# Optimization experiments

Hardware: AMD Instinct MI355X
Metric: run time of the kernel (lower is better)

Reference implementation:

```python
import jax, jax.numpy as jnp
import numpy as np

B, T, N = 2, 256, 512
H, S, C = 64, 8, 8
DYN = 4


def setup_inputs() -> dict:
    key = jax.random.key(0)
    ks = jax.random.split(key, 12)
    sc = 0.05
    return {
        "x": jax.random.normal(ks[0], (B, T, N), jnp.float32),
        "mask": (jax.random.uniform(ks[1], (B, T, N)) < 0.2).astype(jnp.float32),
        "static_context": jax.random.normal(ks[2], (N, S), jnp.float32),
        "node_coords": jax.random.normal(ks[3], (N, C), jnp.float32),
        "W1": jax.random.normal(ks[4], (DYN + S, H), jnp.float32) * sc,
        "b1": jnp.zeros((H,), jnp.float32),
        "W2": jax.random.normal(ks[5], (H, H), jnp.float32) * sc,
        "b2": jnp.zeros((H,), jnp.float32),
        "We1": jax.random.normal(ks[6], (4 * H, H), jnp.float32) * sc,
        "be1": jnp.zeros((H,), jnp.float32),
        "We2": jax.random.normal(ks[7], (H, 1), jnp.float32) * sc,
        "be2": jnp.zeros((1,), jnp.float32),
        "self_loop_logit": jnp.float32(0.5),
        "prior_strength": jnp.float32(1.0),
        "similarity_strength": jnp.float32(1.0),
        "temperature": jnp.float32(0.7),
    }


def reference(x, mask, static_context, node_coords, W1, b1, W2, b2,
              We1, be1, We2, be2, self_loop_logit, prior_strength,
              similarity_strength, temperature):
    Bv, Tv, Nv = x.shape
    # ---- dynamic per-node context over time ----
    observed = 1.0 - mask                                   # [B,T,N]
    count = jnp.maximum(observed.sum(axis=1), 1.0)          # [B,N]
    mean = (x * observed).sum(axis=1) / count               # [B,N]
    centered = (x - mean[:, None, :]) * observed
    std = jnp.sqrt((centered ** 2).sum(axis=1) / count + 1e-6)
    t_idx = jnp.arange(Tv, dtype=x.dtype)[None, :, None]
    latest = jnp.argmax(t_idx * observed, axis=1)           # [B,N] int
    last = jnp.take_along_axis(x, latest[:, None, :], axis=1)[:, 0, :]
    missing_ratio = mask.mean(axis=1)
    dyn = jnp.stack([mean, std, last, missing_ratio], axis=-1)  # [B,N,4]
    # ---- node encoder ----
    static = jnp.broadcast_to(static_context[None], (Bv, Nv, static_context.shape[-1]))
    feats = jnp.concatenate([dyn, static], axis=-1)
    h = jax.nn.relu(feats @ W1 + b1)
    h = jax.nn.relu(h @ W2 + b2)                            # [B,N,H]
    hn = h / jnp.maximum(jnp.linalg.norm(h, axis=-1, keepdims=True), 1e-12)
    # ---- edge MLP on pair features [h_i, h_j, |h_i-h_j|, h_i*h_j] ----
    # split first-layer weight into the four blocks so h_i/h_j terms are O(N)
    Wi, Wj, Wa, Wp = jnp.split(We1, 4, axis=0)              # each [H,H]
    pre_i = h @ Wi                                          # [B,N,H]
    pre_j = h @ Wj
    hi = h[:, :, None, :]                                   # [B,N,1,H]
    hj = h[:, None, :, :]                                   # [B,1,N,H]
    hidden = jax.nn.relu(pre_i[:, :, None, :] + pre_j[:, None, :, :]
                         + jnp.abs(hi - hj) @ Wa + (hi * hj) @ Wp + be1)
    edge_logits = (hidden @ We2 + be2)[..., 0]              # [B,N,N]
    # ---- cosine similarity + distance prior ----
    cos = jnp.einsum('bnh,bmh->bnm', hn, hn)
    eye = jnp.eye(Nv, dtype=x.dtype)
    off = 1.0 - eye
    diff = node_coords[:, None, :] - node_coords[None, :, :]
    dist = jnp.sqrt(jnp.maximum((diff ** 2).sum(-1), 1e-12))
    prior = (1.0 / (1.0 + dist)) * off                      # [N,N]
    # ---- combine, softmax, symmetrize, row-normalize ----
    logits = (edge_logits * off
              + jax.nn.softplus(prior_strength) * prior[None]
              + jax.nn.softplus(similarity_strength) * (cos * off))
    logits = logits + eye[None] * jax.nn.softplus(self_loop_logit)
    temp = jax.nn.softplus(temperature) + 1e-4
    adj = jax.nn.softmax(logits / temp, axis=-1)
    adj = 0.5 * (adj + jnp.swapaxes(adj, -1, -2))
    adj = adj / jnp.maximum(adj.sum(axis=-1, keepdims=True), 1e-6)
    return adj
```

## Files before the change

### kernel.cpp

```cpp
#include <hip/hip_runtime.h>
#include <hip/hip_bf16.h>
#include <math.h>

#define NB 2
#define NT 256
#define NN 512
#define NH 64
#define NS 8
#define NC 8

#define OFF_H      0
#define OFF_PVEC   65536
#define OFF_HF16   131072
#define OFF_HNF16  163840
#define OFF_WA16   196608
#define OFF_WJF    198656
#define OFF_WPF    202752
#define OFF_GBASE  206848
#define OFF_UNSYM  731136

typedef __attribute__((ext_vector_type(8))) _Float16 h8;
typedef __attribute__((ext_vector_type(2))) __fp16 fp16x2;
typedef __attribute__((ext_vector_type(4))) float f32x4;
typedef __attribute__((ext_vector_type(4))) unsigned u4;
typedef __attribute__((ext_vector_type(2))) unsigned u2;

__device__ __forceinline__ float softplusf(float x){
  if (x > 20.f) return x;
  return log1pf(expf(x));
}

__device__ __forceinline__ unsigned pkh(float a, float b){
  fp16x2 h = __builtin_amdgcn_cvt_pkrtz(a, b);
  return __builtin_bit_cast(unsigned, h);
}

template<int CTRL>
__device__ __forceinline__ float dpp_addf(float x){
  int xi = __builtin_bit_cast(int, x);
  int yi = __builtin_amdgcn_update_dpp(0, xi, CTRL, 0xF, 0xF, true);
  return x + __builtin_bit_cast(float, yi);
}
__device__ __forceinline__ float row16_sum(float x){
  x = dpp_addf<0xB1>(x);
  x = dpp_addf<0x4E>(x);
  x = dpp_addf<0x141>(x);
  x = dpp_addf<0x140>(x);
  return x;
}

__global__ __launch_bounds__(256) void k_front(
    const float* __restrict__ x, const float* __restrict__ mask,
    const float* __restrict__ sctx,
    const float* __restrict__ W1, const float* __restrict__ b1,
    const float* __restrict__ W2, const float* __restrict__ b2,
    const float* __restrict__ We1, const float* __restrict__ be1,
    float* __restrict__ hg, float* __restrict__ pvec,
    unsigned* __restrict__ hf16, unsigned* __restrict__ hn16,
    short* __restrict__ wa16, float* __restrict__ wjf,
    float* __restrict__ wpf){
  int blk = blockIdx.x;
  int tid = threadIdx.x;

  if (blk >= 256){
    int pidx = (blk - 256)*256 + tid;
    int e    = pidx & 7;
    int lane = (pidx >> 3) & 63;
    int frag = (pidx >> 9) & 7;
    int nt = frag & 3, ks = frag >> 2;
    int kg = lane >> 4, q = lane & 15;
    int kk = ks*32 + kg*8 + e;
    int c  = nt*16 + q;
    if (pidx < 4096){
      _Float16 v = (_Float16)We1[(128 + kk)*NH + c];
      wa16[pidx] = __builtin_bit_cast(short, v);
    } else if (pidx < 8192){
      wjf[pidx - 4096] = We1[(64 + kk)*NH + c];
    } else {
      wpf[pidx - 8192] = We1[(192 + kk)*NH + c];
    }
    return;
  }

  int b  = blk >> 7;
  int n0 = (blk & 127) * 4;

  int nl = tid & 3;
  int ts = tid >> 2;
  int n  = n0 + nl;

  float cnt = 0.f, sx = 0.f, sxx = 0.f;
  int lastt = 0;
  for (int t = ts*4; t < ts*4 + 4; ++t){
    int idx = (b*NT + t)*NN + n;
    float xv = x[idx];
    float mv = mask[idx];
    bool obs = (mv < 0.5f);
    if (obs){ cnt += 1.f; sx += xv; sxx += xv*xv; lastt = t; }
  }
  #pragma unroll
  for (int m = 4; m < 64; m <<= 1){
    cnt   += __shfl_xor(cnt,  m);
    sx    += __shfl_xor(sx,   m);
    sxx   += __shfl_xor(sxx,  m);
    lastt  = max(lastt, __shfl_xor(lastt, m));
  }
  int w = tid >> 6;
  __shared__ float r_cnt[4][4], r_sx[4][4], r_sxx[4][4];
  __shared__ int   r_lt[4][4];
  __shared__ float s_dyn[4][4];
  if ((tid & 63) < 4){
    r_cnt[w][nl] = cnt; r_sx[w][nl] = sx; r_sxx[w][nl] = sxx; r_lt[w][nl] = lastt;
  }
  __syncthreads();
  if (tid < 4){
    float c = 0.f, s1 = 0.f, s2 = 0.f; int lt = 0;
    #pragma unroll
    for (int ww = 0; ww < 4; ++ww){
      c  += r_cnt[ww][tid]; s1 += r_sx[ww][tid]; s2 += r_sxx[ww][tid];
      lt  = max(lt, r_lt[ww][tid]);
    }
    float cc   = fmaxf(c, 1.f);
    float mean = s1 / cc;
    float var  = s2 / cc - mean*mean;
    float stdv = sqrtf(fmaxf(var, 0.f) + 1e-6f);
    float last = x[(b*NT + lt)*NN + n0 + tid];
    float mr   = 1.f - c * (1.f/(float)NT);
    s_dyn[tid][0] = mean; s_dyn[tid][1] = stdv; s_dyn[tid][2] = last; s_dyn[tid][3] = mr;
  }
  __syncthreads();

  int c = tid & 63;
  int gn = n0 + w;
  int bn = b*NN + gn;
  __shared__ float s_f[4][12];
  __shared__ float s_h1[4][64];
  __shared__ float s_h2[4][64];

  if (c < 4)       s_f[w][c] = s_dyn[w][c];
  else if (c < 12) s_f[w][c] = sctx[gn*NS + (c-4)];
  __syncthreads();

  float a = b1[c];
  #pragma unroll
  for (int k = 0; k < 12; ++k) a = fmaf(s_f[w][k], W1[k*NH + c], a);
  s_h1[w][c] = fmaxf(a, 0.f);
  __syncthreads();

  float a2 = b2[c];
  #pragma unroll 8
  for (int k = 0; k < 64; ++k) a2 = fmaf(s_h1[w][k], W2[k*NH + c], a2);
  a2 = fmaxf(a2, 0.f);

  float sq = a2*a2;
  #pragma unroll
  for (int m = 1; m < 64; m <<= 1) sq += __shfl_xor(sq, m);
  float inv = 1.f / fmaxf(sqrtf(sq), 1e-12f);

  s_h2[w][c] = a2;
  __syncthreads();

  float pi = be1[c];
  #pragma unroll 8
  for (int k = 0; k < 64; ++k) pi = fmaf(s_h2[w][k], We1[k*NH + c], pi);

  hg  [bn*64 + c] = a2;
  pvec[bn*64 + c] = pi;
  if (c < 32){
    float e0 = s_h2[w][2*c], e1 = s_h2[w][2*c + 1];
    hf16[bn*32 + c] = pkh(e0, e1);
    hn16[bn*32 + c] = pkh(e0*inv, e1*inv);
  }
}

__global__ __launch_bounds__(256) void k_gram(
    const unsigned* __restrict__ hn16, const float* __restrict__ s_ss,
    float* __restrict__ gbase){
  int b   = blockIdx.x;
  int i0  = blockIdx.y * 16;
  int jq  = blockIdx.z;
  int tid = threadIdx.x;
  int w   = tid >> 6;
  int lane = tid & 63;
  float spss = softplusf(s_ss[0]);

  const u4* hv = (const u4*)hn16;
  int arow = i0 + (lane & 15);
  u4 a0 = hv[(b*NN + arow)*8 + (lane >> 4)];
  u4 a1 = hv[(b*NN + arow)*8 + (lane >> 4) + 4];
  h8 A0 = __builtin_bit_cast(h8, a0);
  h8 A1 = __builtin_bit_cast(h8, a1);

  #pragma unroll
  for (int t = 0; t < 2; ++t){
    int j0 = (jq*8 + w*2 + t) * 16;
    int jrow = j0 + (lane & 15);
    u4 b0 = hv[(b*NN + jrow)*8 + (lane >> 4)];
    u4 b1 = hv[(b*NN + jrow)*8 + (lane >> 4) + 4];
    f32x4 acc = (f32x4){0.f, 0.f, 0.f, 0.f};
    acc = __builtin_amdgcn_mfma_f32_16x16x32_f16(A0, __builtin_bit_cast(h8, b0), acc, 0, 0, 0);
    acc = __builtin_amdgcn_mfma_f32_16x16x32_f16(A1, __builtin_bit_cast(h8, b1), acc, 0, 0, 0);
    #pragma unroll
    for (int r = 0; r < 4; ++r){
      int irow = i0 + (lane >> 4)*4 + r;
      gbase[(size_t)(b*NN + irow)*NN + j0 + (lane & 15)] = spss * acc[r];
    }
  }
}

__global__ __launch_bounds__(512, 4) void k_logits(
    const float* __restrict__ hg, const float* __restrict__ pvec,
    const unsigned* __restrict__ hf16, const short* __restrict__ wa16,
    const float* __restrict__ wjf, const float* __restrict__ wpf,
    const float* __restrict__ coords, const float* __restrict__ We2,
    const float* __restrict__ be2, const float* __restrict__ gbase,
    const float* __restrict__ s_sl, const float* __restrict__ s_ps,
    const float* __restrict__ s_tp,
    float* __restrict__ unsym){
  int blk = blockIdx.x;
  int b = blk >> 9, i = blk & (NN-1);
  int tid  = threadIdx.x;
  int w    = tid >> 6;
  int lane = tid & 63;
  int q    = lane & 15;
  int kg   = lane >> 4;

  __shared__ __align__(16) float s_hi[64];
  __shared__ __align__(16) float s_pv[64];
  __shared__ __align__(16) float s_prior[NN];
  __shared__ __align__(16) float s_gcos[NN];
  __shared__ __align__(16) float lrow[NN];
  __shared__ __align__(16) unsigned lds_wa[2048];
  __shared__ __align__(16) unsigned lds_cw[2048];
  __shared__ __align__(16) unsigned s_hj[8][16*34 + 2];
  __shared__ float red[16];

  float spsl = softplusf(s_sl[0]);
  float spps = softplusf(s_ps[0]);
  float invt = 1.f / (softplusf(s_tp[0]) + 1e-4f);

  if (tid < 64){
    s_hi[tid] = hg  [(b*NN + i)*64 + tid];
    s_pv[tid] = pvec[(b*NN + i)*64 + tid];
  }
  {
    int j = tid;
    float4 ci0 = *(const float4*)(coords + i*NC);
    float4 ci1 = *(const float4*)(coords + i*NC + 4);
    float4 cj0 = *(const float4*)(coords + j*NC);
    float4 cj1 = *(const float4*)(coords + j*NC + 4);
    float dd = 0.f;
    dd = fmaf(ci0.x-cj0.x, ci0.x-cj0.x, dd);
    dd = fmaf(ci0.y-cj0.y, ci0.y-cj0.y, dd);
    dd = fmaf(ci0.z-cj0.z, ci0.z-cj0.z, dd);
    dd = fmaf(ci0.w-cj0.w, ci0.w-cj0.w, dd);
    dd = fmaf(ci1.x-cj1.x, ci1.x-cj1.x, dd);
    dd = fmaf(ci1.y-cj1.y, ci1.y-cj1.y, dd);
    dd = fmaf(ci1.z-cj1.z, ci1.z-cj1.z, dd);
    dd = fmaf(ci1.w-cj1.w, ci1.w-cj1.w, dd);
    float dist = sqrtf(fmaxf(dd, 1e-12f));
    s_prior[j] = (j == i) ? 0.f : spps / (1.f + dist);
    s_gcos[j]  = gbase[(size_t)(b*NN + i)*NN + j];
  }
  __syncthreads();

  {
    int frag = tid >> 6;
    int l2   = tid & 63;
    const u4* wsrc = (const u4*)wa16;
    *(u4*)&lds_wa[(frag*64 + l2)*4] = wsrc[frag*64 + l2];

    int ch0 = (frag >> 2)*32 + (l2 >> 4)*8;
    const float* wj = wjf + (frag*64 + l2)*8;
    const float* wp = wpf + (frag*64 + l2)*8;
    u4 u;
    #pragma unroll
    for (int d = 0; d < 4; ++d){
      float v0 = fmaf(s_hi[ch0 + 2*d],     wp[2*d],     wj[2*d]);
      float v1 = fmaf(s_hi[ch0 + 2*d + 1], wp[2*d + 1], wj[2*d + 1]);
      u[d] = pkh(v0, v1);
    }
    *(u4*)&lds_cw[(frag*64 + l2)*4] = u;
  }

  const u4* hfv = (const u4*)hf16;
  u4 hi0 = hfv[(b*NN + i)*8 + kg];
  u4 hi1 = hfv[(b*NN + i)*8 + kg + 4];

  float pv4[4], we2q[4];
  #pragma unroll
  for (int nt = 0; nt < 4; ++nt){
    pv4[nt]  = pvec[(b*NN + i)*64 + nt*16 + q];
    we2q[nt] = We2[nt*16 + q];
  }
  float be2v = be2[0];
  __syncthreads();

  unsigned* slice = &s_hj[w][0];
  const u4 absm = (u4){0x7fff7fffu, 0x7fff7fffu, 0x7fff7fffu, 0x7fff7fffu};

  #pragma unroll
  for (int s = 0; s < 4; ++s){
    int it = w + s*8;
    int jbase = it * 16;

    {
      int r8 = lane >> 3, c8 = lane & 7;
      u4 g0 = *(const u4*)((const unsigned*)hf16 + (size_t)(b*NN + jbase + r8)*32 + c8*4);
      u4 g1 = *(const u4*)((const unsigned*)hf16 + (size_t)(b*NN + jbase + 8 + r8)*32 + c8*4);
      unsigned* p0 = slice + r8*34 + c8*4;
      unsigned* p1 = slice + (8 + r8)*34 + c8*4;
      u2 t;
      t.x = g0.x; t.y = g0.y; *(u2*)p0 = t;
      t.x = g0.z; t.y = g0.w; *(u2*)(p0 + 2) = t;
      t.x = g1.x; t.y = g1.y; *(u2*)p1 = t;
      t.x = g1.z; t.y = g1.w; *(u2*)(p1 + 2) = t;
    }

    u4 hj0, hj1;
    {
      unsigned* rp = slice + q*34 + kg*4;
      u2 a0 = *(u2*)rp;
      u2 a1 = *(u2*)(rp + 2);
      u2 b0 = *(u2*)(rp + 16);
      u2 b1 = *(u2*)(rp + 18);
      hj0.x = a0.x; hj0.y = a0.y; hj0.z = a1.x; hj0.w = a1.y;
      hj1.x = b0.x; hj1.y = b0.y; hj1.z = b1.x; hj1.w = b1.y;
    }

    h8 dh0 = __builtin_bit_cast(h8, hi0) - __builtin_bit_cast(h8, hj0);
    h8 dh1 = __builtin_bit_cast(h8, hi1) - __builtin_bit_cast(h8, hj1);
    h8 af0 = __builtin_bit_cast(h8, __builtin_bit_cast(u4, dh0) & absm);
    h8 af1 = __builtin_bit_cast(h8, __builtin_bit_cast(u4, dh1) & absm);
    h8 af2 = __builtin_bit_cast(h8, hj0);
    h8 af3 = __builtin_bit_cast(h8, hj1);

    f32x4 acc[4];
    #pragma unroll
    for (int nt = 0; nt < 4; ++nt)
      acc[nt] = (f32x4){pv4[nt], pv4[nt], pv4[nt], pv4[nt]};
    #pragma unroll
    for (int nt = 0; nt < 4; ++nt){
      h8 wA0 = __builtin_bit_cast(h8, *(const u4*)&lds_wa[((0*4 + nt)*64 + lane)*4]);
      h8 wA1 = __builtin_bit_cast(h8, *(const u4*)&lds_wa[((1*4 + nt)*64 + lane)*4]);
      h8 wC0 = __builtin_bit_cast(h8, *(const u4*)&lds_cw[((0*4 + nt)*64 + lane)*4]);
      h8 wC1 = __builtin_bit_cast(h8, *(const u4*)&lds_cw[((1*4 + nt)*64 + lane)*4]);
      acc[nt] = __builtin_amdgcn_mfma_f32_16x16x32_f16(af0, wA0, acc[nt], 0, 0, 0);
      acc[nt] = __builtin_amdgcn_mfma_f32_16x16x32_f16(af1, wA1, acc[nt], 0, 0, 0);
      acc[nt] = __builtin_amdgcn_mfma_f32_16x16x32_f16(af2, wC0, acc[nt], 0, 0, 0);
      acc[nt] = __builtin_amdgcn_mfma_f32_16x16x32_f16(af3, wC1, acc[nt], 0, 0, 0);
    }

    float part[4] = {0.f, 0.f, 0.f, 0.f};
    #pragma unroll
    for (int nt = 0; nt < 4; ++nt)
      #pragma unroll
      for (int r = 0; r < 4; ++r)
        part[r] = fmaf(fmaxf(acc[nt][r], 0.f), we2q[nt], part[r]);
    #pragma unroll
    for (int r = 0; r < 4; ++r) part[r] = row16_sum(part[r]);

    if (q < 4){
      int j2 = jbase + kg*4 + q;
      float ps2 = part[0];
      ps2 = (q == 1) ? part[1] : ps2;
      ps2 = (q == 2) ? part[2] : ps2;
      ps2 = (q == 3) ? part[3] : ps2;
      float lg = ps2 + be2v + s_prior[j2] + s_gcos[j2];
      lrow[j2] = (j2 == i) ? spsl : lg;
    }
  }
  __syncthreads();

  float v = lrow[tid];
  float m1 = v;
  #pragma unroll
  for (int msk = 1; msk < 64; msk <<= 1) m1 = fmaxf(m1, __shfl_xor(m1, msk));
  if (lane == 0) red[w] = m1;
  __syncthreads();
  m1 = red[0];
  #pragma unroll
  for (int ww = 1; ww < 8; ++ww) m1 = fmaxf(m1, red[ww]);

  float e = expf((v - m1) * invt);
  float se = e;
  #pragma unroll
  for (int msk = 1; msk < 64; msk <<= 1) se += __shfl_xor(se, msk);
  if (lane == 0) red[8 + w] = se;
  __syncthreads();
  se = red[8];
  #pragma unroll
  for (int ww = 1; ww < 8; ++ww) se += red[8 + ww];

  unsym[(size_t)(b*NN + i)*NN + tid] = e / se;
}

__global__ __launch_bounds__(256) void k_sym(
    const float* __restrict__ u, float* __restrict__ out){
  int blk = blockIdx.x;
  int b = blk >> 9, i = blk & (NN-1);
  int tid = threadIdx.x;
  const float* urow = u + (size_t)(b*NN + i) * NN;
  float v0, v1, rs;
  {
    int j0 = tid, j1 = tid + 256;
    float a1 = urow[j0];
    float a2 = u[(size_t)(b*NN + j0) * NN + i];
    v0 = 0.5f*(a1 + a2);
    float a3 = urow[j1];
    float a4 = u[(size_t)(b*NN + j1) * NN + i];
    v1 = 0.5f*(a3 + a4);
    rs = v0 + v1;
  }
  int lane = tid & 63, w = tid >> 6;
  #pragma unroll
  for (int msk = 1; msk < 64; msk <<= 1) rs += __shfl_xor(rs, msk);
  __shared__ float red[4];
  if (lane == 0) red[w] = rs;
  __syncthreads();
  rs = red[0] + red[1] + red[2] + red[3];
  float inv = 1.f / fmaxf(rs, 1e-6f);
  float* orow = out + (size_t)(b*NN + i) * NN;
  orow[tid]       = v0 * inv;
  orow[tid + 256] = v1 * inv;
}

extern "C" void kernel_launch(void* const* d_in, const int* in_sizes, int n_in,
                              void* d_out, int out_size, void* d_ws, size_t ws_size,
                              hipStream_t stream){
  const float* x      = (const float*)d_in[0];
  const float* mask   = (const float*)d_in[1];
  const float* sctx   = (const float*)d_in[2];
  const float* coords = (const float*)d_in[3];
  const float* W1     = (const float*)d_in[4];
  const float* b1     = (const float*)d_in[5];
  const float* W2     = (const float*)d_in[6];
  const float* b2     = (const float*)d_in[7];
  const float* We1    = (const float*)d_in[8];
  const float* be1    = (const float*)d_in[9];
  const float* We2    = (const float*)d_in[10];
  const float* be2    = (const float*)d_in[11];
  const float* sl     = (const float*)d_in[12];
  const float* ps     = (const float*)d_in[13];
  const float* ss     = (const float*)d_in[14];
  const float* tp     = (const float*)d_in[15];

  float*    ws    = (float*)d_ws;
  float*    hgp   = ws + OFF_H;
  float*    pvecp = ws + OFF_PVEC;
  unsigned* hf16p = (unsigned*)(ws + OFF_HF16);
  unsigned* hn16p = (unsigned*)(ws + OFF_HNF16);
  short*    wa16p = (short*)(ws + OFF_WA16);
  float*    wjfp  = ws + OFF_WJF;
  float*    wpfp  = ws + OFF_WPF;
  float*    gbase = ws + OFF_GBASE;
  float*    unsym = ws + OFF_UNSYM;
  float*    out   = (float*)d_out;

  k_front <<<304, 256, 0, stream>>>(x, mask, sctx, W1, b1, W2, b2, We1, be1,
                                    hgp, pvecp, hf16p, hn16p, wa16p, wjfp, wpfp);
  k_gram  <<<dim3(NB, 32, 4), 256, 0, stream>>>(hn16p, ss, gbase);
  k_logits<<<NB*NN, 512, 0, stream>>>(hgp, pvecp, hf16p, wa16p, wjfp, wpfp,
                                      coords, We2, be2, gbase, sl, ps, tp, unsym);
  k_sym   <<<NB*NN, 256, 0, stream>>>(unsym, out);
}
```

Measured before the change: 46.29 us.

## Process two rows per logits block and precompute prior+bias in gram kernel

The logits kernel now handles two query rows per block. Each staged h_j tile and the shared Wa weight fragments are loaded once and reused for both rows, and the block count is halved. The distance prior and edge bias are moved into the gram kernel, which writes one combined additive term per (i,j), so the logits kernel no longer computes coordinates or reads two separate buffers. In exchange there are more registers (two accumulator sets) and more LDS per block, which may lower occupancy and parallelism on a 1024-row problem.

```diff
diff --git a/kernel.cpp b/kernel.cpp
--- a/kernel.cpp
+++ b/kernel.cpp
@@ -16,7 +16,7 @@
 #define OFF_WA16   196608
 #define OFF_WJF    198656
 #define OFF_WPF    202752
-#define OFF_GBASE  206848
+#define OFF_GEXT   206848
 #define OFF_UNSYM  731136
 
 typedef __attribute__((ext_vector_type(8))) _Float16 h8;
@@ -173,9 +173,10 @@
   }
 }
 
-__global__ __launch_bounds__(256) void k_gram(
-    const unsigned* __restrict__ hn16, const float* __restrict__ s_ss,
-    float* __restrict__ gbase){
+__global__ __launch_bounds__(256) void k_extra(
+    const unsigned* __restrict__ hn16, const float* __restrict__ coords,
+    const float* __restrict__ s_ss, const float* __restrict__ s_ps,
+    const float* __restrict__ be2, float* __restrict__ gext){
   int b   = blockIdx.x;
   int i0  = blockIdx.y * 16;
   int jq  = blockIdx.z;
@@ -183,6 +184,8 @@
   int w   = tid >> 6;
   int lane = tid & 63;
   float spss = softplusf(s_ss[0]);
+  float spps = softplusf(s_ps[0]);
+  float be2v = be2[0];
 
   const u4* hv = (const u4*)hn16;
   int arow = i0 + (lane & 15);
@@ -200,10 +203,27 @@
     f32x4 acc = (f32x4){0.f, 0.f, 0.f, 0.f};
     acc = __builtin_amdgcn_mfma_f32_16x16x32_f16(A0, __builtin_bit_cast(h8, b0), acc, 0, 0, 0);
     acc = __builtin_amdgcn_mfma_f32_16x16x32_f16(A1, __builtin_bit_cast(h8, b1), acc, 0, 0, 0);
+
+    int jc = j0 + (lane & 15);
+    float4 cj0 = *(const float4*)(coords + jc*NC);
+    float4 cj1 = *(const float4*)(coords + jc*NC + 4);
     #pragma unroll
     for (int r = 0; r < 4; ++r){
       int irow = i0 + (lane >> 4)*4 + r;
-      gbase[(size_t)(b*NN + irow)*NN + j0 + (lane & 15)] = spss * acc[r];
+      float4 ci0 = *(const float4*)(coords + irow*NC);
+      float4 ci1 = *(const float4*)(coords + irow*NC + 4);
+      float dd = 0.f;
+      dd = fmaf(ci0.x-cj0.x, ci0.x-cj0.x, dd);
+      dd = fmaf(ci0.y-cj0.y, ci0.y-cj0.y, dd);
+      dd = fmaf(ci0.z-cj0.z, ci0.z-cj0.z, dd);
+      dd = fmaf(ci0.w-cj0.w, ci0.w-cj0.w, dd);
+      dd = fmaf(ci1.x-cj1.x, ci1.x-cj1.x, dd);
+      dd = fmaf(ci1.y-cj1.y, ci1.y-cj1.y, dd);
+      dd = fmaf(ci1.z-cj1.z, ci1.z-cj1.z, dd);
+      dd = fmaf(ci1.w-cj1.w, ci1.w-cj1.w, dd);
+      float dist  = sqrtf(fmaxf(dd, 1e-12f));
+      float prior = (irow == jc) ? 0.f : spps / (1.f + dist);
+      gext[(size_t)(b*NN + irow)*NN + jc] = fmaf(spss, acc[r], be2v + prior);
     }
   }
 }
@@ -212,56 +232,34 @@
     const float* __restrict__ hg, const float* __restrict__ pvec,
     const unsigned* __restrict__ hf16, const short* __restrict__ wa16,
     const float* __restrict__ wjf, const float* __restrict__ wpf,
-    const float* __restrict__ coords, const float* __restrict__ We2,
-    const float* __restrict__ be2, const float* __restrict__ gbase,
-    const float* __restrict__ s_sl, const float* __restrict__ s_ps,
-    const float* __restrict__ s_tp,
+    const float* __restrict__ We2, const float* __restrict__ gext,
+    const float* __restrict__ s_sl, const float* __restrict__ s_tp,
     float* __restrict__ unsym){
   int blk = blockIdx.x;
-  int b = blk >> 9, i = blk & (NN-1);
+  int b  = blk >> 8;
+  int ip = (blk & 255) * 2;
   int tid  = threadIdx.x;
   int w    = tid >> 6;
   int lane = tid & 63;
   int q    = lane & 15;
   int kg   = lane >> 4;
 
-  __shared__ __align__(16) float s_hi[64];
-  __shared__ __align__(16) float s_pv[64];
-  __shared__ __align__(16) float s_prior[NN];
-  __shared__ __align__(16) float s_gcos[NN];
-  __shared__ __align__(16) float lrow[NN];
+  __shared__ __align__(16) float s_hi[2][64];
+  __shared__ __align__(16) float s_ext[2][NN];
+  __shared__ __align__(16) float lrow[2][NN];
   __shared__ __align__(16) unsigned lds_wa[2048];
-  __shared__ __align__(16) unsigned lds_cw[2048];
+  __shared__ __align__(16) unsigned lds_cw[2][2048];
   __shared__ __align__(16) unsigned s_hj[8][16*34 + 2];
-  __shared__ float red[16];
+  __shared__ float red[32];
 
   float spsl = softplusf(s_sl[0]);
-  float spps = softplusf(s_ps[0]);
   float invt = 1.f / (softplusf(s_tp[0]) + 1e-4f);
 
-  if (tid < 64){
-    s_hi[tid] = hg  [(b*NN + i)*64 + tid];
-    s_pv[tid] = pvec[(b*NN + i)*64 + tid];
-  }
-  {
-    int j = tid;
-    float4 ci0 = *(const float4*)(coords + i*NC);
-    float4 ci1 = *(const float4*)(coords + i*NC + 4);
-    float4 cj0 = *(const float4*)(coords + j*NC);
-    float4 cj1 = *(const float4*)(coords + j*NC + 4);
-    float dd = 0.f;
-    dd = fmaf(ci0.x-cj0.x, ci0.x-cj0.x, dd);
-    dd = fmaf(ci0.y-cj0.y, ci0.y-cj0.y, dd);
-    dd = fmaf(ci0.z-cj0.z, ci0.z-cj0.z, dd);
-    dd = fmaf(ci0.w-cj0.w, ci0.w-cj0.w, dd);
-    dd = fmaf(ci1.x-cj1.x, ci1.x-cj1.x, dd);
-    dd = fmaf(ci1.y-cj1.y, ci1.y-cj1.y, dd);
-    dd = fmaf(ci1.z-cj1.z, ci1.z-cj1.z, dd);
-    dd = fmaf(ci1.w-cj1.w, ci1.w-cj1.w, dd);
-    float dist = sqrtf(fmaxf(dd, 1e-12f));
-    s_prior[j] = (j == i) ? 0.f : spps / (1.f + dist);
-    s_gcos[j]  = gbase[(size_t)(b*NN + i)*NN + j];
-  }
+  if (tid < 128)
+    s_hi[tid >> 6][tid & 63] = hg[(b*NN + ip + (tid >> 6))*64 + (tid & 63)];
+  #pragma unroll
+  for (int r = 0; r < 2; ++r)
+    s_ext[r][tid] = gext[(size_t)(b*NN + ip + r)*NN + tid];
   __syncthreads();
 
   {
@@ -273,27 +271,35 @@
     int ch0 = (frag >> 2)*32 + (l2 >> 4)*8;
     const float* wj = wjf + (frag*64 + l2)*8;
     const float* wp = wpf + (frag*64 + l2)*8;
-    u4 u;
-    #pragma unroll
-    for (int d = 0; d < 4; ++d){
-      float v0 = fmaf(s_hi[ch0 + 2*d],     wp[2*d],     wj[2*d]);
-      float v1 = fmaf(s_hi[ch0 + 2*d + 1], wp[2*d + 1], wj[2*d + 1]);
-      u[d] = pkh(v0, v1);
-    }
-    *(u4*)&lds_cw[(frag*64 + l2)*4] = u;
+    #pragma unroll
+    for (int r = 0; r < 2; ++r){
+      u4 u;
+      #pragma unroll
+      for (int d = 0; d < 4; ++d){
+        float v0 = fmaf(s_hi[r][ch0 + 2*d],     wp[2*d],     wj[2*d]);
+        float v1 = fmaf(s_hi[r][ch0 + 2*d + 1], wp[2*d + 1], wj[2*d + 1]);
+        u[d] = pkh(v0, v1);
+      }
+      *(u4*)&lds_cw[r][(frag*64 + l2)*4] = u;
+    }
   }
 
   const u4* hfv = (const u4*)hf16;
-  u4 hi0 = hfv[(b*NN + i)*8 + kg];
-  u4 hi1 = hfv[(b*NN + i)*8 + kg + 4];
-
-  float pv4[4], we2q[4];
+  u4 hiA[2][2];
+  #pragma unroll
+  for (int r = 0; r < 2; ++r){
+    hiA[r][0] = hfv[(b*NN + ip + r)*8 + kg];
+    hiA[r][1] = hfv[(b*NN + ip + r)*8 + kg + 4];
+  }
+
+  float pv4[2][4], we2q[4];
   #pragma unroll
   for (int nt = 0; nt < 4; ++nt){
-    pv4[nt]  = pvec[(b*NN + i)*64 + nt*16 + q];
+    #pragma unroll
+    for (int r = 0; r < 2; ++r)
+      pv4[r][nt] = pvec[(b*NN + ip + r)*64 + nt*16 + q];
     we2q[nt] = We2[nt*16 + q];
   }
-  float be2v = be2[0];
   __syncthreads();
 
   unsigned* slice = &s_hj[w][0];
@@ -327,72 +333,94 @@
       hj0.x = a0.x; hj0.y = a0.y; hj0.z = a1.x; hj0.w = a1.y;
       hj1.x = b0.x; hj1.y = b0.y; hj1.z = b1.x; hj1.w = b1.y;
     }
-
-    h8 dh0 = __builtin_bit_cast(h8, hi0) - __builtin_bit_cast(h8, hj0);
-    h8 dh1 = __builtin_bit_cast(h8, hi1) - __builtin_bit_cast(h8, hj1);
-    h8 af0 = __builtin_bit_cast(h8, __builtin_bit_cast(u4, dh0) & absm);
-    h8 af1 = __builtin_bit_cast(h8, __builtin_bit_cast(u4, dh1) & absm);
-    h8 af2 = __builtin_bit_cast(h8, hj0);
-    h8 af3 = __builtin_bit_cast(h8, hj1);
-
-    f32x4 acc[4];
-    #pragma unroll
-    for (int nt = 0; nt < 4; ++nt)
-      acc[nt] = (f32x4){pv4[nt], pv4[nt], pv4[nt], pv4[nt]};
+    h8 hjv0 = __builtin_bit_cast(h8, hj0);
+    h8 hjv1 = __builtin_bit_cast(h8, hj1);
+
+    f32x4 acc[2][4];
+    #pragma unroll
+    for (int r = 0; r < 2; ++r)
+      #pragma unroll
+      for (int nt = 0; nt < 4; ++nt)
+        acc[r][nt] = (f32x4){pv4[r][nt], pv4[r][nt], pv4[r][nt], pv4[r][nt]};
+
     #pragma unroll
     for (int nt = 0; nt < 4; ++nt){
       h8 wA0 = __builtin_bit_cast(h8, *(const u4*)&lds_wa[((0*4 + nt)*64 + lane)*4]);
       h8 wA1 = __builtin_bit_cast(h8, *(const u4*)&lds_wa[((1*4 + nt)*64 + lane)*4]);
-      h8 wC0 = __builtin_bit_cast(h8, *(const u4*)&lds_cw[((0*4 + nt)*64 + lane)*4]);
-      h8 wC1 = __builtin_bit_cast(h8, *(const u4*)&lds_cw[((1*4 + nt)*64 + lane)*4]);
-      acc[nt] = __builtin_amdgcn_mfma_f32_16x16x32_f16(af0, wA0, acc[nt], 0, 0, 0);
-      acc[nt] = __builtin_amdgcn_mfma_f32_16x16x32_f16(af1, wA1, acc[nt], 0, 0, 0);
-      acc[nt] = __builtin_amdgcn_mfma_f32_16x16x32_f16(af2, wC0, acc[nt], 0, 0, 0);
-      acc[nt] = __builtin_amdgcn_mfma_f32_16x16x32_f16(af3, wC1, acc[nt], 0, 0, 0);
-    }
-
-    float part[4] = {0.f, 0.f, 0.f, 0.f};
-    #pragma unroll
-    for (int nt = 0; nt < 4; ++nt)
       #pragma unroll
-      for (int r = 0; r < 4; ++r)
-        part[r] = fmaf(fmaxf(acc[nt][r], 0.f), we2q[nt], part[r]);
-    #pragma unroll
-    for (int r = 0; r < 4; ++r) part[r] = row16_sum(part[r]);
-
-    if (q < 4){
-      int j2 = jbase + kg*4 + q;
-      float ps2 = part[0];
-      ps2 = (q == 1) ? part[1] : ps2;
-      ps2 = (q == 2) ? part[2] : ps2;
-      ps2 = (q == 3) ? part[3] : ps2;
-      float lg = ps2 + be2v + s_prior[j2] + s_gcos[j2];
-      lrow[j2] = (j2 == i) ? spsl : lg;
-    }
-  }
-  __syncthreads();
-
-  float v = lrow[tid];
-  float m1 = v;
-  #pragma unroll
-  for (int msk = 1; msk < 64; msk <<= 1) m1 = fmaxf(m1, __shfl_xor(m1, msk));
-  if (lane == 0) red[w] = m1;
-  __syncthreads();
-  m1 = red[0];
-  #pragma unroll
-  for (int ww = 1; ww < 8; ++ww) m1 = fmaxf(m1, red[ww]);
-
-  float e = expf((v - m1) * invt);
-  float se = e;
-  #pragma unroll
-  for (int msk = 1; msk < 64; msk <<= 1) se += __shfl_xor(se, msk);
-  if (lane == 0) red[8 + w] = se;
-  __syncthreads();
-  se = red[8];
-  #pragma unroll
-  for (int ww = 1; ww < 8; ++ww) se += red[8 + ww];
-
-  unsym[(size_t)(b*NN + i)*NN + tid] = e / se;
+      for (int r = 0; r < 2; ++r){
+        h8 dh0 = __builtin_bit_cast(h8, hiA[r][0]) - hjv0;
+        h8 dh1 = __builtin_bit_cast(h8, hiA[r][1]) - hjv1;
+        h8 af0 = __builtin_bit_cast(h8, __builtin_bit_cast(u4, dh0) & absm);
+        h8 af1 = __builtin_bit_cast(h8, __builtin_bit_cast(u4, dh1) & absm);
+        h8 wC0 = __builtin_bit_cast(h8, *(const u4*)&lds_cw[r][((0*4 + nt)*64 + lane)*4]);
+        h8 wC1 = __builtin_bit_cast(h8, *(const u4*)&lds_cw[r][((1*4 + nt)*64 + lane)*4]);
+        acc[r][nt] = __builtin_amdgcn_mfma_f32_16x16x32_f16(af0, wA0, acc[r][nt], 0, 0, 0);
+        acc[r][nt] = __builtin_amdgcn_mfma_f32_16x16x32_f16(af1, wA1, acc[r][nt], 0, 0, 0);
+        acc[r][nt] = __builtin_amdgcn_mfma_f32_16x16x32_f16(hjv0, wC0, acc[r][nt], 0, 0, 0);
+        acc[r][nt] = __builtin_amdgcn_mfma_f32_16x16x32_f16(hjv1, wC1, acc[r][nt], 0, 0, 0);
+      }
+    }
+
+    #pragma unroll
+    for (int r = 0; r < 2; ++r){
+      float part[4] = {0.f, 0.f, 0.f, 0.f};
+      #pragma unroll
+      for (int nt = 0; nt < 4; ++nt)
+        #pragma unroll
+        for (int rr = 0; rr < 4; ++rr)
+          part[rr] = fmaf(fmaxf(acc[r][nt][rr], 0.f), we2q[nt], part[rr]);
+      #pragma unroll
+      for (int rr = 0; rr < 4; ++rr) part[rr] = row16_sum(part[rr]);
+
+      if (q < 4){
+        int j2 = jbase + kg*4 + q;
+        float ps2 = part[0];
+        ps2 = (q == 1) ? part[1] : ps2;
+        ps2 = (q == 2) ? part[2] : ps2;
+        ps2 = (q == 3) ? part[3] : ps2;
+        float lg = ps2 + s_ext[r][j2];
+        lrow[r][j2] = (j2 == ip + r) ? spsl : lg;
+      }
+    }
+  }
+  __syncthreads();
+
+  float va = lrow[0][tid], vb = lrow[1][tid];
+  float ma = va, mb = vb;
+  #pragma unroll
+  for (int msk = 1; msk < 64; msk <<= 1){
+    ma = fmaxf(ma, __shfl_xor(ma, msk));
+    mb = fmaxf(mb, __shfl_xor(mb, msk));
+  }
+  if (lane == 0){ red[w] = ma; red[8 + w] = mb; }
+  __syncthreads();
+  ma = red[0]; mb = red[8];
+  #pragma unroll
+  for (int ww = 1; ww < 8; ++ww){
+    ma = fmaxf(ma, red[ww]);
+    mb = fmaxf(mb, red[8 + ww]);
+  }
+
+  float ea = expf((va - ma) * invt);
+  float eb = expf((vb - mb) * invt);
+  float sa = ea, sb = eb;
+  #pragma unroll
+  for (int msk = 1; msk < 64; msk <<= 1){
+    sa += __shfl_xor(sa, msk);
+    sb += __shfl_xor(sb, msk);
+  }
+  if (lane == 0){ red[16 + w] = sa; red[24 + w] = sb; }
+  __syncthreads();
+  sa = red[16]; sb = red[24];
+  #pragma unroll
+  for (int ww = 1; ww < 8; ++ww){
+    sa += red[16 + ww];
+    sb += red[24 + ww];
+  }
+
+  unsym[(size_t)(b*NN + ip)*NN + tid]       = ea / sa;
+  unsym[(size_t)(b*NN + ip + 1)*NN + tid]   = eb / sb;
 }
 
 __global__ __launch_bounds__(256) void k_sym(
@@ -453,14 +481,14 @@
   short*    wa16p = (short*)(ws + OFF_WA16);
   float*    wjfp  = ws + OFF_WJF;
   float*    wpfp  = ws + OFF_WPF;
-  float*    gbase = ws + OFF_GBASE;
+  float*    gext  = ws + OFF_GEXT;
   float*    unsym = ws + OFF_UNSYM;
   float*    out   = (float*)d_out;
 
   k_front <<<304, 256, 0, stream>>>(x, mask, sctx, W1, b1, W2, b2, We1, be1,
                                     hgp, pvecp, hf16p, hn16p, wa16p, wjfp, wpfp);
-  k_gram  <<<dim3(NB, 32, 4), 256, 0, stream>>>(hn16p, ss, gbase);
-  k_logits<<<NB*NN, 512, 0, stream>>>(hgp, pvecp, hf16p, wa16p, wjfp, wpfp,
-                                      coords, We2, be2, gbase, sl, ps, tp, unsym);
+  k_extra <<<dim3(NB, 32, 4), 256, 0, stream>>>(hn16p, coords, ss, ps, be2, gext);
+  k_logits<<<NB*NN/2, 512, 0, stream>>>(hgp, pvecp, hf16p, wa16p, wjfp, wpfp,
+                                        We2, gext, sl, tp, unsym);
   k_sym   <<<NB*NN, 256, 0, stream>>>(unsym, out);
 }
```

Result: faster. 43.61 us (-5.8%).
